# Kernel optimization log

Hardware: AMD Instinct MI355X
Metric: run time of the kernel (lower is better)

The kernel has to match this reference:

```python
import jax, jax.numpy as jnp
import numpy as np

N, CIN, T, V, P, K, NCLS = 8, 3, 300, 25, 3, 9, 60
EPS = 1e-5


def setup_inputs() -> dict:
    key = jax.random.key(0)
    ks = jax.random.split(key, 10)
    rn = lambda k, s: jax.random.normal(k, s, jnp.float32) * 0.05
    return {
        "x": jax.random.normal(ks[0], (N, CIN, T, V), jnp.float32),
        "A": jax.random.uniform(ks[1], (P, V, V), jnp.float32),
        "bn_in_g": jnp.ones((V * CIN,), jnp.float32),
        "bn_in_b": jnp.zeros((V * CIN,), jnp.float32),
        "fin_W": rn(ks[2], (64, CIN)), "fin_b": jnp.zeros((64,), jnp.float32),
        "imp0": jnp.ones((V, V), jnp.float32), "imp1": jnp.ones((V, V), jnp.float32),
        "imp2": jnp.ones((V, V), jnp.float32), "imp3": jnp.ones((V, V), jnp.float32),
        "W0": rn(ks[3], (64 * P, 64)), "g0": jnp.ones((64,), jnp.float32), "b0": jnp.zeros((64,), jnp.float32),
        "W1": rn(ks[4], (128 * P, 64)), "g1": jnp.ones((128,), jnp.float32), "b1": jnp.zeros((128,), jnp.float32),
        "Wr1": rn(ks[5], (128, 64)), "gr1": jnp.ones((128,), jnp.float32), "br1": jnp.zeros((128,), jnp.float32),
        "W2": rn(ks[6], (256 * P, 128)), "g2": jnp.ones((256,), jnp.float32), "b2": jnp.zeros((256,), jnp.float32),
        "Wr2": rn(ks[7], (256, 128)), "gr2": jnp.ones((256,), jnp.float32), "br2": jnp.zeros((256,), jnp.float32),
        "W3": rn(ks[8], (256 * P, 256)), "g3": jnp.ones((256,), jnp.float32), "b3": jnp.zeros((256,), jnp.float32),
        "fout_W": rn(ks[9], (NCLS, 256)), "fout_b": jnp.zeros((NCLS,), jnp.float32),
    }


def _bn(x, g, b, axes):
    # training-mode batchnorm (batch statistics), matching nn.BatchNorm in train()
    m = jnp.mean(x, axes, keepdims=True)
    v = jnp.var(x, axes, keepdims=True)
    return (x - m) * jax.lax.rsqrt(v + EPS) * g + b


def _lt_matrix(t):
    # lower-triangular-style shift matrix: lt[r, c] = 1 iff 0 <= c - r < K (stride 1)
    d = jnp.arange(t)[None, :] - jnp.arange(t)[:, None]
    return ((d >= 0) & (d < K)).astype(jnp.float32)


def _layer(x, A, W, g, b, lt, res, final_relu):
    # x: (N, Cin, T, V); W: (P*Cout, Cin); A: (P, V, V); lt: (T, T)
    n, _, t, v = x.shape
    cout = W.shape[0] // P
    y = jnp.einsum('nctv,kc->nktv', x, W).reshape(n, P, cout, t, v)   # 1x1 conv + split/stack
    z = jnp.einsum('npctv,pvw->npctw', y, A)                          # spatial graph matmul
    u = jnp.einsum('npctv,ts->npcsv', z, lt)                          # dense LxL temporal matmul
    h = u.sum(1)                                                      # sum over partitions -> (N, Cout, T, V)
    h = jax.nn.relu(_bn(h, g[None, :, None, None], b[None, :, None, None], (0, 2, 3)))
    out = h + res
    return jax.nn.relu(out) if final_relu else out


def reference(x, A, bn_in_g, bn_in_b, fin_W, fin_b, imp0, imp1, imp2, imp3,
              W0, g0, b0, W1, g1, b1, Wr1, gr1, br1,
              W2, g2, b2, Wr2, gr2, br2, W3, g3, b3, fout_W, fout_b):
    n, c, t, v = x.shape
    # input BatchNorm1d over (V*C) channels
    xp = x.transpose(0, 3, 1, 2).reshape(n, v * c, t)
    xp = _bn(xp, bn_in_g[None, :, None], bn_in_b[None, :, None], (0, 2))
    h = xp.reshape(n, v, c, t).transpose(0, 2, 3, 1)                  # (N, C, T, V)
    h = jnp.einsum('nctv,oc->notv', h, fin_W) + fin_b[None, :, None, None]
    lt = _lt_matrix(t)
    # layer 0: no residual, no final relu (Dropout only, p=0 -> identity)
    h = _layer(h, A * imp0, W0, g0, b0, lt, 0.0, False)
    # layer 1: 64 -> 128, conv+BN residual
    r1 = _bn(jnp.einsum('nctv,oc->notv', h, Wr1), gr1[None, :, None, None], br1[None, :, None, None], (0, 2, 3))
    h = _layer(h, A * imp1, W1, g1, b1, lt, r1, True)
    # layer 2: 128 -> 256, conv+BN residual
    r2 = _bn(jnp.einsum('nctv,oc->notv', h, Wr2), gr2[None, :, None, None], br2[None, :, None, None], (0, 2, 3))
    h = _layer(h, A * imp2, W2, g2, b2, lt, r2, True)
    # layer 3: 256 -> 256, identity residual
    h = _layer(h, A * imp3, W3, g3, b3, lt, h, True)
    # average pool over joints, 1x1 classification conv
    h = h.mean(-1, keepdims=True)                                     # (N, 256, T, 1)
    out = jnp.einsum('nctv,oc->notv', h, fout_W) + fout_b[None, :, None, None]
    return out[..., 0]                                                # (N, num_classes, T)
```

## Files before the change

### kernel.cpp

```cpp
#include <hip/hip_runtime.h>

#define EPS 1e-5f
typedef unsigned short u16;
typedef __attribute__((ext_vector_type(8))) short short8;
typedef __attribute__((ext_vector_type(4))) float f32x4;

__device__ __forceinline__ float bf2f(u16 u) {
  union { unsigned int i; float f; } c; c.i = ((unsigned int)u) << 16; return c.f;
}
__device__ __forceinline__ u16 f2bf(float f) {
  union { float f; unsigned int i; } c; c.f = f;
  unsigned int u = c.i;
  u += 0x7fffu + ((u >> 16) & 1u);
  return (u16)(u >> 16);
}
__device__ __forceinline__ float bits2f(unsigned int b) {
  union { unsigned int i; float f; } c; c.i = b; return c.f;
}
__device__ __forceinline__ unsigned int cvt_pk_bf16(float lo, float hi) {
  unsigned int r;
  asm("v_cvt_pk_bf16_f32 %0, %1, %2" : "=v"(r) : "v"(lo), "v"(hi));
  return r;
}
__device__ __forceinline__ short8 load8u(const u16* p) {
  short8 v; __builtin_memcpy(&v, p, 16); return v;
}
__device__ __forceinline__ void gload16(const u16* g, u16* l) {
  __builtin_amdgcn_global_load_lds(
      (__attribute__((address_space(1))) void*)(void*)g,
      (__attribute__((address_space(3))) void*)l, 16, 0, 0);
}

__device__ __forceinline__ void prep_w_elem(const float* W, u16* Wt,
    int cin, int cout, int P, int idx) {
  const int K = P*cin;
  const int co = idx / K, k = idx % K;
  const int p = k / cin, ci = k % cin;
  Wt[idx] = f2bf(W[((size_t)(p*cout + co))*cin + ci]);
}

__global__ __launch_bounds__(256) void k_prep_all(
    const float* __restrict__ A,
    const float* __restrict__ i0, const float* __restrict__ i1,
    const float* __restrict__ i2, const float* __restrict__ i3,
    const float* __restrict__ W0, const float* __restrict__ W1,
    const float* __restrict__ Wr1, const float* __restrict__ W2,
    const float* __restrict__ Wr2, const float* __restrict__ W3,
    float* __restrict__ Ap, u16* W0t, u16* W1t, u16* Wr1t, u16* W2t,
    u16* Wr2t, u16* W3t, u16* ATb, u16* hpad) {
  int idx = blockIdx.x*256 + threadIdx.x;
  if (idx < 7500) {
    const int layer = idx / 1875, r = idx % 1875;
    const int vw = r % 625;
    const float* imp = (layer==0)?i0:(layer==1)?i1:(layer==2)?i2:i3;
    Ap[idx] = A[r] * imp[vw];
    return;
  }
  idx -= 7500;
  if (idx < 12288) { prep_w_elem(W0,  W0t,  64,  64,  3, idx); return; }
  idx -= 12288;
  if (idx < 24576) { prep_w_elem(W1,  W1t,  64,  128, 3, idx); return; }
  idx -= 24576;
  if (idx < 8192)  { prep_w_elem(Wr1, Wr1t, 64,  128, 1, idx); return; }
  idx -= 8192;
  if (idx < 98304) { prep_w_elem(W2,  W2t,  128, 256, 3, idx); return; }
  idx -= 98304;
  if (idx < 32768) { prep_w_elem(Wr2, Wr2t, 128, 256, 1, idx); return; }
  idx -= 32768;
  if (idx < 196608){ prep_w_elem(W3,  W3t,  256, 256, 3, idx); return; }
  idx -= 196608;
  if (idx < 12288) {
    const int l = idx / 3072, r = idx % 3072;
    const int p = r / 1024, wv = r % 1024;
    const int w = wv >> 5, v = wv & 31;
    float val = 0.f;
    if (w < 25 && v < 25) {
      const float* imp = (l==0)?i0:(l==1)?i1:(l==2)?i2:i3;
      val = A[(p*25 + v)*25 + w] * imp[v*25 + w];
    }
    ATb[idx] = f2bf(val);
    return;
  }
  idx -= 12288;
  if (idx < 32) hpad[idx] = 0;
}

__global__ __launch_bounds__(256) void k_bn_in_stats(const float* __restrict__ x,
    const float* __restrict__ g, const float* __restrict__ b,
    float* __restrict__ iscale, float* __restrict__ ishift) {
  const int j = blockIdx.x;
  const int c = j % 3, v = j / 3;
  const int tid = threadIdx.x;
  float s = 0.f, q = 0.f;
  for (int i = tid; i < 2400; i += 256) {
    const int n = i / 300, t = i % 300;
    const float val = x[(((size_t)n*3 + c)*300 + t)*25 + v];
    s += val; q += val*val;
  }
  __shared__ float rs[256], rq[256];
  rs[tid] = s; rq[tid] = q;
  __syncthreads();
  for (int off = 128; off > 0; off >>= 1) {
    if (tid < off) { rs[tid] += rs[tid+off]; rq[tid] += rq[tid+off]; }
    __syncthreads();
  }
  if (tid == 0) {
    const float mean = rs[0] / 2400.f;
    const float var  = rq[0] / 2400.f - mean*mean;
    const float sc = g[j] * rsqrtf(var + EPS);
    iscale[j] = sc;
    ishift[j] = b[j] - mean*sc;
  }
}

__global__ __launch_bounds__(256) void k_fin(const float* __restrict__ x,
    const float* __restrict__ iscale, const float* __restrict__ ishift,
    const float* __restrict__ fW, const float* __restrict__ fb,
    u16* __restrict__ H) {
  const int n = blockIdx.y;
  const int t0 = blockIdx.x * 10;
  const int tid = threadIdx.x;
  __shared__ float xn[3][250];
  __shared__ float wsh[64][3];
  __shared__ float bsh[64];
  if (tid < 192) wsh[tid/3][tid%3] = fW[tid];
  if (tid < 64)  bsh[tid] = fb[tid];
  for (int i = tid; i < 750; i += 256) {
    const int c = i / 250, pos = i % 250;
    const int t = t0 + pos/25, v = pos%25;
    const int j = v*3 + c;
    xn[c][pos] = x[(((size_t)n*3 + c)*300 + t)*25 + v] * iscale[j] + ishift[j];
  }
  __syncthreads();
  for (int e = tid; e < 64*250; e += 256) {
    const int o = e / 250, pos = e % 250;
    float acc = bsh[o]
              + xn[0][pos]*wsh[o][0] + xn[1][pos]*wsh[o][1] + xn[2][pos]*wsh[o][2];
    const int t = t0 + pos/25, v = pos%25;
    H[(((size_t)n*64 + o)*300 + t)*25 + v] = f2bf(acc);
  }
}

__global__ __launch_bounds__(256) void k_xa_mfma(const u16* __restrict__ H,
    const u16* __restrict__ ATl, u16* __restrict__ XA, int cin, int K) {
  const int lane = threadIdx.x & 63, wid = threadIdx.x >> 6;
  const int t = blockIdx.x * 4 + wid;
  const int n = blockIdx.y;
  const int lrow = lane & 15, lchunk = lane >> 4;
  short8 bf[3][2];
  #pragma unroll
  for (int p = 0; p < 3; ++p)
    #pragma unroll
    for (int wt = 0; wt < 2; ++wt)
      bf[p][wt] = *(const short8*)&ATl[(p*32 + wt*16 + lrow)*32 + lchunk*8];
  const int ntile = cin >> 4;
  const size_t mrow0 = ((size_t)n*300 + t)*25;
  const int ciq = lchunk*4;
  for (int citile = 0; citile < ntile; ++citile) {
    const int ci = citile*16 + lrow;
    const short8 af = load8u(&H[((size_t)(n*cin + ci)*300 + t)*25 + lchunk*8]);
    #pragma unroll
    for (int p = 0; p < 3; ++p) {
      #pragma unroll
      for (int wt = 0; wt < 2; ++wt) {
        f32x4 acc = (f32x4){0.f, 0.f, 0.f, 0.f};
        acc = __builtin_amdgcn_mfma_f32_16x16x32_bf16(af, bf[p][wt], acc, 0, 0, 0);
        const int w = wt*16 + lrow;
        if (w < 25) {
          uint2 pk;
          pk.x = cvt_pk_bf16(acc[0], acc[1]);
          pk.y = cvt_pk_bf16(acc[2], acc[3]);
          *(uint2*)&XA[(mrow0 + w)*K + p*cin + citile*16 + ciq] = pk;
        }
      }
    }
  }
}

__global__ __launch_bounds__(256) void k_xa3(const u16* __restrict__ H,
    const float* __restrict__ Ap, u16* __restrict__ XA, u16* Hmk,
    int cin, int log2cin) {
  const int t0 = blockIdx.x * 2;
  const int n  = blockIdx.y;
  const int tid = threadIdx.x;
  const int K = 3 * cin;
  extern __shared__ unsigned int xs[];
  float* As = (float*)(xs + cin*27);

  for (int i = tid; i < 1875; i += 256) {
    const int p = i / 625, r = i % 625;
    As[p*700 + (r/25)*28 + (r%25)] = Ap[i];
  }
  for (int idx = tid; idx < cin*25; idx += 256) {
    const int ci = idx / 25, c = idx % 25;
    const char* src = (const char*)H + ((((size_t)n*cin + ci)*7500) + (size_t)t0*25)*2 + c*4;
    xs[ci*27 + c] = *(const unsigned int*)src;
  }
  __syncthreads();

  for (int kc = 0; kc < K; kc += 256) {
    const int k = kc + tid;
    if (k < K) {
      const int ci = k & (cin - 1);
      const int p  = k >> log2cin;
      const float* __restrict__ Ab = &As[p*700];

      unsigned int raw[25];
      #pragma unroll
      for (int j = 0; j < 25; ++j) raw[j] = xs[ci*27 + j];

      float acc0[25], acc1[25];
      #pragma unroll
      for (int w = 0; w < 25; ++w) { acc0[w] = 0.f; acc1[w] = 0.f; }

      #pragma unroll
      for (int v = 0; v < 25; ++v) {
        const int e1 = 25 + v;
        const float xv0 = bits2f((v & 1)  ? (raw[v  >> 1] & 0xffff0000u)
                                          : (raw[v  >> 1] << 16));
        const float xv1 = bits2f((e1 & 1) ? (raw[e1 >> 1] & 0xffff0000u)
                                          : (raw[e1 >> 1] << 16));
        #pragma unroll
        for (int j = 0; j < 7; ++j) {
          const f32x4 a = *(const f32x4*)&Ab[v*28 + j*4];
          #pragma unroll
          for (int e = 0; e < 4; ++e) {
            const int w = j*4 + e;
            if (w < 25) {
              acc0[w] = fmaf(a[e], xv0, acc0[w]);
              acc1[w] = fmaf(a[e], xv1, acc1[w]);
            }
          }
        }
      }

      const size_t mb0 = ((size_t)n*300 + t0)*25;
      #pragma unroll
      for (int w = 0; w < 25; ++w) XA[(mb0 + w)*K + k]      = f2bf(acc0[w]);
      #pragma unroll
      for (int w = 0; w < 25; ++w) XA[(mb0 + 25 + w)*K + k] = f2bf(acc1[w]);

      if (p == 0) {
        #pragma unroll
        for (int v = 0; v < 25; ++v) {
          const unsigned int b0 = (v & 1) ? (raw[v >> 1] >> 16) : (raw[v >> 1] & 0xffffu);
          Hmk[(mb0 + v)*cin + ci] = (u16)b0;
        }
        #pragma unroll
        for (int v = 0; v < 25; ++v) {
          const int e = 25 + v;
          const unsigned int b1 = (e & 1) ? (raw[e >> 1] >> 16) : (raw[e >> 1] & 0xffffu);
          Hmk[(mb0 + 25 + v)*cin + ci] = (u16)b1;
        }
      }
    }
  }
}

__global__ __launch_bounds__(256) void k_gemm(const u16* __restrict__ Asrc,
    const u16* __restrict__ Bsrc, u16* __restrict__ Cb, int K) {
  const int n0b = blockIdx.x * 64;
  const int m0  = blockIdx.y * 128;
  const int tid = threadIdx.x;
  const int lane = tid & 63, wid = tid >> 6;
  const int wm = (wid & 1) * 64, wn = (wid >> 1) * 32;

  __shared__ u16 As[128*64];
  __shared__ u16 Bs[64*64];

  f32x4 acc[4][2];
  #pragma unroll
  for (int mi = 0; mi < 4; ++mi)
    #pragma unroll
    for (int ni = 0; ni < 2; ++ni) acc[mi][ni] = (f32x4){0.f,0.f,0.f,0.f};

  const int rA = tid >> 3, cA = tid & 7;

  const int nkt = K >> 6;
  for (int kt = 0; kt < nkt; ++kt) {
    const int kbase = kt * 64;
    __syncthreads();
    #pragma unroll
    for (int i = 0; i < 4; ++i) {
      const int idx = tid + i*256;
      const int r = rA + i*32;
      int m = m0 + r; if (m > 59999) m = 59999;
      gload16(Asrc + (size_t)m*K + kbase + ((cA ^ (r & 7)) * 8), &As[idx*8]);
    }
    #pragma unroll
    for (int i = 0; i < 2; ++i) {
      const int idx = tid + i*256;
      const int r = rA + i*32;
      gload16(Bsrc + (size_t)(n0b + r)*K + kbase + ((cA ^ (r & 7)) * 8), &Bs[idx*8]);
    }
    __syncthreads();
    #pragma unroll
    for (int kc = 0; kc < 2; ++kc) {
      const int kchunk = kc*4 + (lane >> 4);
      short8 a[4], b[2];
      #pragma unroll
      for (int mi = 0; mi < 4; ++mi) {
        const int m = wm + mi*16 + (lane & 15);
        a[mi] = *(const short8*)&As[m*64 + ((kchunk ^ (m & 7)) * 8)];
      }
      #pragma unroll
      for (int ni = 0; ni < 2; ++ni) {
        const int r = wn + ni*16 + (lane & 15);
        b[ni] = *(const short8*)&Bs[r*64 + ((kchunk ^ (r & 7)) * 8)];
      }
      #pragma unroll
      for (int mi = 0; mi < 4; ++mi)
        #pragma unroll
        for (int ni = 0; ni < 2; ++ni)
          acc[mi][ni] = __builtin_amdgcn_mfma_f32_16x16x32_bf16(a[mi], b[ni], acc[mi][ni], 0, 0, 0);
    }
  }

  const int mrow = (lane >> 4) * 4;
  #pragma unroll
  for (int mi = 0; mi < 4; ++mi) {
    const int mb = m0 + wm + mi*16 + mrow;
    if (mb >= 60000) continue;
    #pragma unroll
    for (int ni = 0; ni < 2; ++ni) {
      const int co = n0b + wn + ni*16 + (lane & 15);
      uint2 pk;
      pk.x = cvt_pk_bf16(acc[mi][ni][0], acc[mi][ni][1]);
      pk.y = cvt_pk_bf16(acc[mi][ni][2], acc[mi][ni][3]);
      *(uint2*)&Cb[(size_t)co*60000 + mb] = pk;
    }
  }
}

__global__ __launch_bounds__(512) void k_gemm2(const u16* __restrict__ Asrc,
    const u16* __restrict__ Bsrc, u16* __restrict__ Cb, int K) {
  const int m0 = blockIdx.x * 128;
  const int tid = threadIdx.x;
  const int lane = tid & 63, wid = tid >> 6;
  const int wm = (wid >> 2) * 64, wn = (wid & 3) * 64;

  __shared__ u16 As[128*64];
  __shared__ u16 Bs[256*64];

  f32x4 acc[4][4];
  #pragma unroll
  for (int mi = 0; mi < 4; ++mi)
    #pragma unroll
    for (int ni = 0; ni < 4; ++ni) acc[mi][ni] = (f32x4){0.f,0.f,0.f,0.f};

  const int rA = tid >> 3, cA = tid & 7;

  const int nkt = K >> 6;
  for (int kt = 0; kt < nkt; ++kt) {
    const int kbase = kt * 64;
    __syncthreads();
    #pragma unroll
    for (int i = 0; i < 2; ++i) {
      const int idx = tid + i*512;
      const int r = rA + i*64;
      int m = m0 + r; if (m > 59999) m = 59999;
      gload16(Asrc + (size_t)m*K + kbase + ((cA ^ (r & 7)) * 8), &As[idx*8]);
    }
    #pragma unroll
    for (int i = 0; i < 4; ++i) {
      const int idx = tid + i*512;
      const int r = rA + i*64;
      gload16(Bsrc + (size_t)r*K + kbase + ((cA ^ (r & 7)) * 8), &Bs[idx*8]);
    }
    __syncthreads();
    #pragma unroll
    for (int kc = 0; kc < 2; ++kc) {
      const int kchunk = kc*4 + (lane >> 4);
      short8 a[4], b[4];
      #pragma unroll
      for (int mi = 0; mi < 4; ++mi) {
        const int m = wm + mi*16 + (lane & 15);
        a[mi] = *(const short8*)&As[m*64 + ((kchunk ^ (m & 7)) * 8)];
      }
      #pragma unroll
      for (int ni = 0; ni < 4; ++ni) {
        const int r = wn + ni*16 + (lane & 15);
        b[ni] = *(const short8*)&Bs[r*64 + ((kchunk ^ (r & 7)) * 8)];
      }
      #pragma unroll
      for (int mi = 0; mi < 4; ++mi)
        #pragma unroll
        for (int ni = 0; ni < 4; ++ni)
          acc[mi][ni] = __builtin_amdgcn_mfma_f32_16x16x32_bf16(a[mi], b[ni], acc[mi][ni], 0, 0, 0);
    }
  }

  const int mrow = (lane >> 4) * 4;
  #pragma unroll
  for (int mi = 0; mi < 4; ++mi) {
    const int mb = m0 + wm + mi*16 + mrow;
    if (mb >= 60000) continue;
    #pragma unroll
    for (int ni = 0; ni < 4; ++ni) {
      const int co = wn + ni*16 + (lane & 15);
      uint2 pk;
      pk.x = cvt_pk_bf16(acc[mi][ni][0], acc[mi][ni][1]);
      pk.y = cvt_pk_bf16(acc[mi][ni][2], acc[mi][ni][3]);
      *(uint2*)&Cb[(size_t)co*60000 + mb] = pk;
    }
  }
}

__global__ __launch_bounds__(256) void k_bn_part_win(const u16* __restrict__ G,
    float* __restrict__ part, int cout) {
  const int c = blockIdx.x, n = blockIdx.y;
  const int tid = threadIdx.x;
  const u16* gb = G + (size_t)c*60000 + (size_t)n*7500;
  float s = 0.f, q = 0.f;
  for (int i = tid; i < 7500; i += 256) {
    const int ss = i / 25, w = i % 25;
    float S = 0.f;
    if (ss >= 8) {
      #pragma unroll
      for (int d = 0; d < 9; ++d) S += bf2f(gb[i - d*25]);
    } else {
      for (int tt = 0; tt <= ss; ++tt) S += bf2f(gb[tt*25 + w]);
    }
    s += S; q += S*S;
  }
  __shared__ float rs[256], rq[256];
  rs[tid] = s; rq[tid] = q;
  __syncthreads();
  for (int off = 128; off > 0; off >>= 1) {
    if (tid < off) { rs[tid] += rs[tid+off]; rq[tid] += rq[tid+off]; }
    __syncthreads();
  }
  if (tid == 0) {
    part[((size_t)c*8 + n)*2]     = rs[0];
    part[((size_t)c*8 + n)*2 + 1] = rq[0];
  }
}

__global__ __launch_bounds__(256) void k_bn_part_plain(const u16* __restrict__ R,
    float* __restrict__ part, int cout) {
  const int c = blockIdx.x, n = blockIdx.y;
  const int tid = threadIdx.x;
  const u16* rb = R + (size_t)c*60000 + (size_t)n*7500;
  float s = 0.f, q = 0.f;
  for (int i = tid; i < 7500; i += 256) {
    const float val = bf2f(rb[i]);
    s += val; q += val*val;
  }
  __shared__ float rs[256], rq[256];
  rs[tid] = s; rq[tid] = q;
  __syncthreads();
  for (int off = 128; off > 0; off >>= 1) {
    if (tid < off) { rs[tid] += rs[tid+off]; rq[tid] += rq[tid+off]; }
    __syncthreads();
  }
  if (tid == 0) {
    part[((size_t)c*8 + n)*2]     = rs[0];
    part[((size_t)c*8 + n)*2 + 1] = rq[0];
  }
}

__global__ __launch_bounds__(256) void k_apply2(const u16* __restrict__ G,
    const u16* __restrict__ Rb, const u16* Hres,
    const float* __restrict__ part, const float* __restrict__ g, const float* __restrict__ b,
    const float* __restrict__ rpart, const float* __restrict__ rg, const float* __restrict__ rbb,
    u16* Out, int cout, int mode) {
  const int bc = blockIdx.x;
  const int c = bc % cout, n = bc / cout;
  float s = 0.f, q = 0.f;
  #pragma unroll
  for (int i = 0; i < 8; ++i) {
    s += part[((size_t)c*8 + i)*2];
    q += part[((size_t)c*8 + i)*2 + 1];
  }
  const float mean = s / 60000.f;
  const float var  = q / 60000.f - mean*mean;
  const float sc = g[c] * rsqrtf(var + EPS);
  const float sh = b[c] - mean*sc;
  float rsc = 0.f, rsh = 0.f;
  if (mode == 1) {
    float s2 = 0.f, q2 = 0.f;
    #pragma unroll
    for (int i = 0; i < 8; ++i) {
      s2 += rpart[((size_t)c*8 + i)*2];
      q2 += rpart[((size_t)c*8 + i)*2 + 1];
    }
    const float m2 = s2 / 60000.f;
    const float v2 = q2 / 60000.f - m2*m2;
    rsc = rg[c] * rsqrtf(v2 + EPS);
    rsh = rbb[c] - m2*rsc;
  }
  const u16* gb = G + (size_t)c*60000 + (size_t)n*7500;
  const size_t rbase = (size_t)c*60000 + (size_t)n*7500;
  for (int i = threadIdx.x; i < 7500; i += 256) {
    const int ss = i / 25, w = i % 25;
    float S = 0.f;
    if (ss >= 8) {
      #pragma unroll
      for (int d = 0; d < 9; ++d) S += bf2f(gb[i - d*25]);
    } else {
      for (int tt = 0; tt <= ss; ++tt) S += bf2f(gb[tt*25 + w]);
    }
    const float h = fmaxf(S*sc + sh, 0.f);
    float o;
    if (mode == 0)      o = h;
    else if (mode == 1) o = fmaxf(h + (bf2f(Rb[rbase + i])*rsc + rsh), 0.f);
    else                o = fmaxf(h + bf2f(Hres[(size_t)bc*7500 + i]), 0.f);
    Out[(size_t)bc*7500 + i] = f2bf(o);
  }
}

__global__ void k_pool(const u16* __restrict__ H, float* __restrict__ HP) {
  const int idx = blockIdx.x*256 + threadIdx.x;
  if (idx >= 8*256*300) return;
  const u16* base = H + (size_t)idx * 25;
  float s = 0.f;
  #pragma unroll
  for (int v = 0; v < 25; ++v) s += bf2f(base[v]);
  HP[idx] = s * (1.f/25.f);
}

__global__ __launch_bounds__(256) void k_fout(const float* __restrict__ HP,
    const float* __restrict__ fW, const float* __restrict__ fb,
    float* __restrict__ out) {
  const int n = blockIdx.y;
  const int t0 = blockIdx.x * 32;
  const int tid = threadIdx.x;
  __shared__ float hp[256][32];
  for (int i = tid; i < 256*32; i += 256) {
    const int c = i / 32, tt = i % 32;
    const int t = t0 + tt;
    hp[c][tt] = (t < 300) ? HP[((size_t)n*256 + c)*300 + t] : 0.f;
  }
  __syncthreads();
  for (int e = tid; e < 60*32; e += 256) {
    const int o = e / 32, tt = e % 32;
    const int t = t0 + tt;
    if (t >= 300) continue;
    float acc = fb[o];
    for (int c = 0; c < 256; ++c) acc += hp[c][tt] * fW[o*256 + c];
    out[((size_t)n*60 + o)*300 + t] = acc;
  }
}

extern "C" void kernel_launch(void* const* d_in, const int* in_sizes, int n_in,
                              void* d_out, int out_size, void* d_ws, size_t ws_size,
                              hipStream_t stream) {
  (void)in_sizes; (void)n_in; (void)out_size; (void)ws_size;
  const float* x     = (const float*)d_in[0];
  const float* A     = (const float*)d_in[1];
  const float* bng   = (const float*)d_in[2];
  const float* bnb   = (const float*)d_in[3];
  const float* finW  = (const float*)d_in[4];
  const float* finb  = (const float*)d_in[5];
  const float* imp0  = (const float*)d_in[6];
  const float* imp1  = (const float*)d_in[7];
  const float* imp2  = (const float*)d_in[8];
  const float* imp3  = (const float*)d_in[9];
  const float* W0    = (const float*)d_in[10];
  const float* g0    = (const float*)d_in[11];
  const float* b0    = (const float*)d_in[12];
  const float* W1    = (const float*)d_in[13];
  const float* g1    = (const float*)d_in[14];
  const float* b1    = (const float*)d_in[15];
  const float* Wr1   = (const float*)d_in[16];
  const float* gr1   = (const float*)d_in[17];
  const float* br1   = (const float*)d_in[18];
  const float* W2    = (const float*)d_in[19];
  const float* g2    = (const float*)d_in[20];
  const float* b2    = (const float*)d_in[21];
  const float* Wr2   = (const float*)d_in[22];
  const float* gr2   = (const float*)d_in[23];
  const float* br2   = (const float*)d_in[24];
  const float* W3    = (const float*)d_in[25];
  const float* g3    = (const float*)d_in[26];
  const float* b3    = (const float*)d_in[27];
  const float* foutW = (const float*)d_in[28];
  const float* foutb = (const float*)d_in[29];
  float* out = (float*)d_out;

  char* base = (char*)d_ws;
  u16*   Z    = (u16*)base;
  u16*   Hmk  = (u16*)base;
  float* HP   = (float*)(base + 40000000);
  float* PART = (float*)(base + 45000000);
  float* RPART= (float*)(base + 45100000);
  u16*   XA   = (u16*)(base + 61440000);
  u16*   Rb   = (u16*)(base + 107520000);
  u16*   Hct  = (u16*)(base + 153600000);
  u16*   HPAD = (u16*)(base + 184320000);
  u16*   ATb  = (u16*)(base + 185000000);
  u16*   WT   = (u16*)(base + 186777600);
  float* Ap   = (float*)(base + 187523072);
  float* ST   = Ap + 7500;
  float* ISC = ST, *ISH = ST + 80;

  u16* W0t  = WT;
  u16* W1t  = WT + 12288;
  u16* Wr1t = WT + 36864;
  u16* W2t  = WT + 45056;
  u16* Wr2t = WT + 143360;
  u16* W3t  = WT + 176128;

  k_prep_all<<<1534, 256, 0, stream>>>(A, imp0, imp1, imp2, imp3,
      W0, W1, Wr1, W2, Wr2, W3, Ap, W0t, W1t, Wr1t, W2t, Wr2t, W3t, ATb, HPAD);

  k_bn_in_stats<<<75, 256, 0, stream>>>(x, bng, bnb, ISC, ISH);
  k_fin<<<dim3(30, 8), 256, 0, stream>>>(x, ISC, ISH, finW, finb, Hct);

  const int lds64  = (64*27  + 2100) * 4;
  const int lds128 = (128*27 + 2100) * 4;
  const int MT = 469;

  k_xa_mfma<<<dim3(75, 8), 256, 0, stream>>>(Hct, ATb, XA, 64, 192);
  k_gemm<<<dim3(1, MT), 256, 0, stream>>>(XA, W0t, Z, 192);
  k_bn_part_win<<<dim3(64, 8), 256, 0, stream>>>(Z, PART, 64);
  k_apply2<<<8*64, 256, 0, stream>>>(Z, nullptr, nullptr, PART, g0, b0,
      nullptr, nullptr, nullptr, Hct, 64, 0);

  k_xa3<<<dim3(150, 8), 256, lds64, stream>>>(Hct, Ap + 1875, XA, Hmk, 64, 6);
  k_gemm<<<dim3(2, MT), 256, 0, stream>>>(Hmk, Wr1t, Rb, 64);
  k_bn_part_plain<<<dim3(128, 8), 256, 0, stream>>>(Rb, RPART, 128);
  k_gemm<<<dim3(2, MT), 256, 0, stream>>>(XA, W1t, Z, 192);
  k_bn_part_win<<<dim3(128, 8), 256, 0, stream>>>(Z, PART, 128);
  k_apply2<<<8*128, 256, 0, stream>>>(Z, Rb, nullptr, PART, g1, b1,
      RPART, gr1, br1, Hct, 128, 1);

  k_xa3<<<dim3(150, 8), 256, lds128, stream>>>(Hct, Ap + 3750, XA, Hmk, 128, 7);
  k_gemm2<<<MT, 512, 0, stream>>>(Hmk, Wr2t, Rb, 128);
  k_bn_part_plain<<<dim3(256, 8), 256, 0, stream>>>(Rb, RPART, 256);
  k_gemm2<<<MT, 512, 0, stream>>>(XA, W2t, Z, 384);
  k_bn_part_win<<<dim3(256, 8), 256, 0, stream>>>(Z, PART, 256);
  k_apply2<<<8*256, 256, 0, stream>>>(Z, Rb, nullptr, PART, g2, b2,
      RPART, gr2, br2, Hct, 256, 1);

  k_xa_mfma<<<dim3(75, 8), 256, 0, stream>>>(Hct, ATb + 3*3072, XA, 256, 768);
  k_gemm2<<<MT, 512, 0, stream>>>(XA, W3t, Z, 768);
  k_bn_part_win<<<dim3(256, 8), 256, 0, stream>>>(Z, PART, 256);
  k_apply2<<<8*256, 256, 0, stream>>>(Z, nullptr, Hct, PART, g3, b3,
      nullptr, nullptr, nullptr, Hct, 256, 2);

  k_pool<<<2400, 256, 0, stream>>>(Hct, HP);
  k_fout<<<dim3(10, 8), 256, 0, stream>>>(HP, foutW, foutb, out);
}
```

Baseline: 480.7 us.

## Replace scalar k_xa3 with MFMA graph mix plus separate transpose kernel

Layers 1 and 2 now compute the graph-adjacency mixing with the existing MFMA-based k_xa_mfma kernel instead of the scalar FMA k_xa3 kernel. The position-major copy of the activations needed by the residual GEMM is produced by a new LDS-tiled transpose kernel. The fp32 A*imp prep is dropped from k_prep_all because the bf16 ATb tables are used instead. This trades scalar fp32 arithmetic for matrix-core throughput, at the cost of one extra launch and an extra read of H per layer.

```diff
diff --git a/kernel.cpp b/kernel.cpp
--- a/kernel.cpp
+++ b/kernel.cpp
@@ -13,9 +13,6 @@
   unsigned int u = c.i;
   u += 0x7fffu + ((u >> 16) & 1u);
   return (u16)(u >> 16);
-}
-__device__ __forceinline__ float bits2f(unsigned int b) {
-  union { unsigned int i; float f; } c; c.i = b; return c.f;
 }
 __device__ __forceinline__ unsigned int cvt_pk_bf16(float lo, float hi) {
   unsigned int r;
@@ -46,17 +43,9 @@
     const float* __restrict__ W0, const float* __restrict__ W1,
     const float* __restrict__ Wr1, const float* __restrict__ W2,
     const float* __restrict__ Wr2, const float* __restrict__ W3,
-    float* __restrict__ Ap, u16* W0t, u16* W1t, u16* Wr1t, u16* W2t,
+    u16* W0t, u16* W1t, u16* Wr1t, u16* W2t,
     u16* Wr2t, u16* W3t, u16* ATb, u16* hpad) {
   int idx = blockIdx.x*256 + threadIdx.x;
-  if (idx < 7500) {
-    const int layer = idx / 1875, r = idx % 1875;
-    const int vw = r % 625;
-    const float* imp = (layer==0)?i0:(layer==1)?i1:(layer==2)?i2:i3;
-    Ap[idx] = A[r] * imp[vw];
-    return;
-  }
-  idx -= 7500;
   if (idx < 12288) { prep_w_elem(W0,  W0t,  64,  64,  3, idx); return; }
   idx -= 12288;
   if (idx < 24576) { prep_w_elem(W1,  W1t,  64,  128, 3, idx); return; }
@@ -141,6 +130,38 @@
   }
 }
 
+__global__ __launch_bounds__(256) void k_hmk(const u16* __restrict__ H,
+    u16* __restrict__ Hmk, int cin) {
+  const int m0  = blockIdx.x * 64;
+  const int ci0 = blockIdx.y * 32;
+  const int n   = blockIdx.z;
+  __shared__ u16 tile[32][72];
+  const int tid = threadIdx.x;
+  {
+    const int ci = tid >> 3, chunk = tid & 7;
+    const int m = m0 + chunk * 8;
+    const u16* src = &H[(size_t)(n*cin + ci0 + ci)*7500];
+    short8 v;
+    if (m + 7 < 7500) {
+      v = load8u(&src[m]);
+    } else {
+      #pragma unroll
+      for (int j = 0; j < 8; ++j)
+        ((u16*)&v)[j] = (m + j < 7500) ? src[m + j] : (u16)0;
+    }
+    *(short8*)&tile[ci][chunk*8] = v;
+  }
+  __syncthreads();
+  const int mr = tid >> 2, cq = (tid & 3) * 8;
+  const int m = m0 + mr;
+  if (m < 7500) {
+    short8 v;
+    #pragma unroll
+    for (int j = 0; j < 8; ++j) ((u16*)&v)[j] = tile[cq + j][mr];
+    *(short8*)&Hmk[((size_t)n*7500 + m)*cin + ci0 + cq] = v;
+  }
+}
+
 __global__ __launch_bounds__(256) void k_xa_mfma(const u16* __restrict__ H,
     const u16* __restrict__ ATl, u16* __restrict__ XA, int cin, int K) {
   const int lane = threadIdx.x & 63, wid = threadIdx.x >> 6;
@@ -171,86 +192,6 @@
           pk.x = cvt_pk_bf16(acc[0], acc[1]);
           pk.y = cvt_pk_bf16(acc[2], acc[3]);
           *(uint2*)&XA[(mrow0 + w)*K + p*cin + citile*16 + ciq] = pk;
-        }
-      }
-    }
-  }
-}
-
-__global__ __launch_bounds__(256) void k_xa3(const u16* __restrict__ H,
-    const float* __restrict__ Ap, u16* __restrict__ XA, u16* Hmk,
-    int cin, int log2cin) {
-  const int t0 = blockIdx.x * 2;
-  const int n  = blockIdx.y;
-  const int tid = threadIdx.x;
-  const int K = 3 * cin;
-  extern __shared__ unsigned int xs[];
-  float* As = (float*)(xs + cin*27);
-
-  for (int i = tid; i < 1875; i += 256) {
-    const int p = i / 625, r = i % 625;
-    As[p*700 + (r/25)*28 + (r%25)] = Ap[i];
-  }
-  for (int idx = tid; idx < cin*25; idx += 256) {
-    const int ci = idx / 25, c = idx % 25;
-    const char* src = (const char*)H + ((((size_t)n*cin + ci)*7500) + (size_t)t0*25)*2 + c*4;
-    xs[ci*27 + c] = *(const unsigned int*)src;
-  }
-  __syncthreads();
-
-  for (int kc = 0; kc < K; kc += 256) {
-    const int k = kc + tid;
-    if (k < K) {
-      const int ci = k & (cin - 1);
-      const int p  = k >> log2cin;
-      const float* __restrict__ Ab = &As[p*700];
-
-      unsigned int raw[25];
-      #pragma unroll
-      for (int j = 0; j < 25; ++j) raw[j] = xs[ci*27 + j];
-
-      float acc0[25], acc1[25];
-      #pragma unroll
-      for (int w = 0; w < 25; ++w) { acc0[w] = 0.f; acc1[w] = 0.f; }
-
-      #pragma unroll
-      for (int v = 0; v < 25; ++v) {
-        const int e1 = 25 + v;
-        const float xv0 = bits2f((v & 1)  ? (raw[v  >> 1] & 0xffff0000u)
-                                          : (raw[v  >> 1] << 16));
-        const float xv1 = bits2f((e1 & 1) ? (raw[e1 >> 1] & 0xffff0000u)
-                                          : (raw[e1 >> 1] << 16));
-        #pragma unroll
-        for (int j = 0; j < 7; ++j) {
-          const f32x4 a = *(const f32x4*)&Ab[v*28 + j*4];
-          #pragma unroll
-          for (int e = 0; e < 4; ++e) {
-            const int w = j*4 + e;
-            if (w < 25) {
-              acc0[w] = fmaf(a[e], xv0, acc0[w]);
-              acc1[w] = fmaf(a[e], xv1, acc1[w]);
-            }
-          }
-        }
-      }
-
-      const size_t mb0 = ((size_t)n*300 + t0)*25;
-      #pragma unroll
-      for (int w = 0; w < 25; ++w) XA[(mb0 + w)*K + k]      = f2bf(acc0[w]);
-      #pragma unroll
-      for (int w = 0; w < 25; ++w) XA[(mb0 + 25 + w)*K + k] = f2bf(acc1[w]);
-
-      if (p == 0) {
-        #pragma unroll
-        for (int v = 0; v < 25; ++v) {
-          const unsigned int b0 = (v & 1) ? (raw[v >> 1] >> 16) : (raw[v >> 1] & 0xffffu);
-          Hmk[(mb0 + v)*cin + ci] = (u16)b0;
-        }
-        #pragma unroll
-        for (int v = 0; v < 25; ++v) {
-          const int e = 25 + v;
-          const unsigned int b1 = (e & 1) ? (raw[e >> 1] >> 16) : (raw[e >> 1] & 0xffffu);
-          Hmk[(mb0 + 25 + v)*cin + ci] = (u16)b1;
         }
       }
     }
@@ -590,8 +531,7 @@
   u16*   HPAD = (u16*)(base + 184320000);
   u16*   ATb  = (u16*)(base + 185000000);
   u16*   WT   = (u16*)(base + 186777600);
-  float* Ap   = (float*)(base + 187523072);
-  float* ST   = Ap + 7500;
+  float* ST   = (float*)(base + 188000000);
   float* ISC = ST, *ISH = ST + 80;
 
   u16* W0t  = WT;
@@ -601,14 +541,12 @@
   u16* Wr2t = WT + 143360;
   u16* W3t  = WT + 176128;
 
-  k_prep_all<<<1534, 256, 0, stream>>>(A, imp0, imp1, imp2, imp3,
-      W0, W1, Wr1, W2, Wr2, W3, Ap, W0t, W1t, Wr1t, W2t, Wr2t, W3t, ATb, HPAD);
+  k_prep_all<<<1505, 256, 0, stream>>>(A, imp0, imp1, imp2, imp3,
+      W0, W1, Wr1, W2, Wr2, W3, W0t, W1t, Wr1t, W2t, Wr2t, W3t, ATb, HPAD);
 
   k_bn_in_stats<<<75, 256, 0, stream>>>(x, bng, bnb, ISC, ISH);
   k_fin<<<dim3(30, 8), 256, 0, stream>>>(x, ISC, ISH, finW, finb, Hct);
 
-  const int lds64  = (64*27  + 2100) * 4;
-  const int lds128 = (128*27 + 2100) * 4;
   const int MT = 469;
 
   k_xa_mfma<<<dim3(75, 8), 256, 0, stream>>>(Hct, ATb, XA, 64, 192);
@@ -617,7 +555,8 @@
   k_apply2<<<8*64, 256, 0, stream>>>(Z, nullptr, nullptr, PART, g0, b0,
       nullptr, nullptr, nullptr, Hct, 64, 0);
 
-  k_xa3<<<dim3(150, 8), 256, lds64, stream>>>(Hct, Ap + 1875, XA, Hmk, 64, 6);
+  k_hmk<<<dim3(118, 2, 8), 256, 0, stream>>>(Hct, Hmk, 64);
+  k_xa_mfma<<<dim3(75, 8), 256, 0, stream>>>(Hct, ATb + 1*3072, XA, 64, 192);
   k_gemm<<<dim3(2, MT), 256, 0, stream>>>(Hmk, Wr1t, Rb, 64);
   k_bn_part_plain<<<dim3(128, 8), 256, 0, stream>>>(Rb, RPART, 128);
   k_gemm<<<dim3(2, MT), 256, 0, stream>>>(XA, W1t, Z, 192);
@@ -625,7 +564,8 @@
   k_apply2<<<8*128, 256, 0, stream>>>(Z, Rb, nullptr, PART, g1, b1,
       RPART, gr1, br1, Hct, 128, 1);
 
-  k_xa3<<<dim3(150, 8), 256, lds128, stream>>>(Hct, Ap + 3750, XA, Hmk, 128, 7);
+  k_hmk<<<dim3(118, 4, 8), 256, 0, stream>>>(Hct, Hmk, 128);
+  k_xa_mfma<<<dim3(75, 8), 256, 0, stream>>>(Hct, ATb + 2*3072, XA, 128, 384);
   k_gemm2<<<MT, 512, 0, stream>>>(Hmk, Wr2t, Rb, 128);
   k_bn_part_plain<<<dim3(256, 8), 256, 0, stream>>>(Rb, RPART, 256);
   k_gemm2<<<MT, 512, 0, stream>>>(XA, W2t, Z, 384);
```

Result: no change. 473.7 us (-1.5%).
